# Performance work log

Measured on AMD Instinct MI355X. Metric: run time of the kernel, lower is better.

The kernel has to match this reference:

```python
import jax, jax.numpy as jnp
import numpy as np

EPS = 1e-5  # equinox LayerNorm default eps

def setup_inputs() -> dict:
    key = jax.random.key(0)
    k1, k2, k3, k4, k5 = jax.random.split(key, 5)
    heads, d, dH, N = 16, 1024, 64, 2048
    # lecun-normal-ish scaling for fan_in=d
    s = 1.0 / np.sqrt(d)
    return {
        "x": jax.random.normal(k1, (d, N), dtype=jnp.float32),
        "WQ": jax.random.normal(k2, (heads, d, dH), dtype=jnp.float32) * s,
        "WK": jax.random.normal(k3, (heads, d, dH), dtype=jnp.float32) * s,
        "WV": jax.random.normal(k4, (heads, d, dH), dtype=jnp.float32) * s,
        "W0": jax.random.normal(k5, (d, d), dtype=jnp.float32) * s,
    }

def reference(x, WQ, WK, WV, W0):
    # x: [d, N]
    residual = x
    # equinox LayerNorm over full shape (d, N), no affine params
    mean = jnp.mean(x)
    var = jnp.var(x)
    xn = (x - mean) * jax.lax.rsqrt(var + EPS)
    # project: [h, d_model, dH] x [d_model, N] -> [h, dH, N]
    Q = jnp.einsum('hcd,ci->hdi', WQ, xn)
    K = jnp.einsum('hcd,ci->hdi', WK, xn)
    V = jnp.einsum('hcd,ci->hdi', WV, xn)
    dH = WK.shape[-1]
    dot = jnp.einsum('hdi,hdj->hij', Q, K)  # [h, N, N]
    alpha = jax.nn.softmax(dot / jnp.sqrt(jnp.asarray(dH, dot.dtype)), axis=-1)
    attn = jnp.einsum('hij,hdj->hdi', alpha, V)  # [h, dH, N]
    N = attn.shape[2]
    attn = attn.reshape(-1, N)  # [d, N]
    out = W0 @ attn
    return out + residual
```

## Files before the change

### kernel.cpp

```cpp
#include <hip/hip_runtime.h>
#include <math.h>

typedef unsigned short u16;
typedef _Float16 f16;
typedef __attribute__((ext_vector_type(8))) short bf16x8;
typedef __attribute__((ext_vector_type(4))) float f32x4;
typedef __attribute__((ext_vector_type(4))) f16 f16x4;

#define D_MODEL 1024
#define SEQ_N   2048
#define HEADS   16
#define DHEAD   64
#define M3      3072
#define JSPLIT  2
#define JCHUNK  (SEQ_N / JSPLIT)
#define NIT     (JCHUNK / 64)

#define GLOBAL_AS __attribute__((address_space(1)))
#define LDS_AS    __attribute__((address_space(3)))
#define ASYNC16(gp, lp) __builtin_amdgcn_global_load_lds( \
    (const GLOBAL_AS unsigned int*)(gp), (LDS_AS unsigned int*)(lp), 16, 0, 0)

__device__ __forceinline__ u16 f2bf(float f) {
  union { float f; unsigned int u; } v; v.f = f;
  unsigned int r = v.u + 0x7fffu + ((v.u >> 16) & 1u);
  return (u16)(r >> 16);
}

__global__ __launch_bounds__(256) void ln_reduce1(const float* __restrict__ x,
                                                  double* __restrict__ part, int n4) {
  const float4* x4 = (const float4*)x;
  double s = 0.0, ss = 0.0;
  for (int idx = blockIdx.x * blockDim.x + threadIdx.x; idx < n4;
       idx += gridDim.x * blockDim.x) {
    float4 v = x4[idx];
    s  += (double)v.x + (double)v.y + (double)v.z + (double)v.w;
    ss += (double)v.x * v.x + (double)v.y * v.y + (double)v.z * v.z + (double)v.w * v.w;
  }
  __shared__ double ls[256], lss[256];
  int t = threadIdx.x;
  ls[t] = s; lss[t] = ss;
  __syncthreads();
  for (int off = 128; off > 0; off >>= 1) {
    if (t < off) { ls[t] += ls[t + off]; lss[t] += lss[t + off]; }
    __syncthreads();
  }
  if (t == 0) { part[2 * blockIdx.x] = ls[0]; part[2 * blockIdx.x + 1] = lss[0]; }
}

__global__ __launch_bounds__(256) void ln_norm_t(const float* __restrict__ x,
                                                 const double* __restrict__ part,
                                                 u16* __restrict__ xnt) {
  __shared__ double ls[256], lss[256];
  __shared__ float tile[64][65];
  int t = threadIdx.x;
  ls[t] = part[2 * t]; lss[t] = part[2 * t + 1];
  __syncthreads();
  for (int off = 128; off > 0; off >>= 1) {
    if (t < off) { ls[t] += ls[t + off]; lss[t] += lss[t + off]; }
    __syncthreads();
  }
  double inv = 1.0 / ((double)D_MODEL * (double)SEQ_N);
  double m = ls[0] * inv;
  double vv = lss[0] * inv - m * m;
  float mean = (float)m;
  float rstd = (float)(1.0 / sqrt(vv + 1e-5));

  int ib = blockIdx.x * 64, cb = blockIdx.y * 64;
  int il = t & 63, cl = t >> 6;
  for (int r = 0; r < 16; ++r) {
    int c = cl + r * 4;
    tile[c][il] = (x[(size_t)(cb + c) * SEQ_N + ib + il] - mean) * rstd;
  }
  __syncthreads();
  int c2 = t & 63, i2 = t >> 6;
  for (int r = 0; r < 16; ++r) {
    int i = i2 + r * 4;
    xnt[(size_t)(ib + i) * D_MODEL + cb + c2] = f2bf(tile[c2][i]);
  }
}

__global__ __launch_bounds__(256) void pack_w(const float* __restrict__ WQ,
                                              const float* __restrict__ WK,
                                              const float* __restrict__ WV,
                                              const float* __restrict__ W0,
                                              u16* __restrict__ Wp,
                                              u16* __restrict__ W0p) {
  int t = threadIdx.x;
  if (blockIdx.z == 3) {
    int flat = blockIdx.y * (D_MODEL / 32) + blockIdx.x;
    int idx = flat * 512 + t;
#pragma unroll
    for (int r = 0; r < 2; ++r, idx += 256) {
      float4 v = ((const float4*)W0)[idx];
      unsigned int lo = (unsigned int)f2bf(v.x) | ((unsigned int)f2bf(v.y) << 16);
      unsigned int hi = (unsigned int)f2bf(v.z) | ((unsigned int)f2bf(v.w) << 16);
      uint2 o; o.x = lo; o.y = hi;
      *(uint2*)(&W0p[(size_t)idx * 4]) = o;
    }
    return;
  }
  __shared__ float tile[32][65];
  const float* W = (blockIdx.z == 0) ? WQ : ((blockIdx.z == 1) ? WK : WV);
  int h = blockIdx.y, cb = blockIdx.x * 32;
  int dh = t & 63, cl = t >> 6;
  for (int r = 0; r < 8; ++r) {
    int c = cl + r * 4;
    tile[c][dh] = W[((size_t)h * D_MODEL + cb + c) * DHEAD + dh];
  }
  __syncthreads();
  int c2 = t & 31, d2 = t >> 5;
  for (int r = 0; r < 8; ++r) {
    int dd = d2 + r * 8;
    Wp[(size_t)((blockIdx.z * HEADS + h) * DHEAD + dd) * D_MODEL + cb + c2] =
        f2bf(tile[c2][dd]);
  }
}

__global__ __launch_bounds__(256) void gemm_qkv(const u16* __restrict__ A,
                                                const u16* __restrict__ Bt,
                                                u16* __restrict__ Qt,
                                                u16* __restrict__ Kt,
                                                f16* __restrict__ Vb) {
  __shared__ __align__(16) u16 Alds[2 * 96 * 32];
  __shared__ __align__(16) u16 Blds[2 * 128 * 32];
  int t = threadIdx.x;
  int lane = t & 63, w = t >> 6;
  int g = lane >> 4, l16 = lane & 15;
  int wr = w >> 1, wc = w & 1;
  int mb = blockIdx.y * 96, nb = blockIdx.x * 128;

  f32x4 acc[3][4];
#pragma unroll
  for (int i = 0; i < 3; ++i)
#pragma unroll
    for (int j = 0; j < 4; ++j) acc[i][j] = (f32x4){0.f, 0.f, 0.f, 0.f};

  const u16* AgP[3]; int ldsA[3];
#pragma unroll
  for (int r = 0; r < 3; ++r) {
    int idx = r * 256 + t;
    int kk = (idx >= 384) ? 1 : 0;
    int rem = idx - kk * 384;
    int row = rem >> 2, c4 = rem & 3;
    AgP[r] = A + (size_t)(mb + row) * D_MODEL + kk * 32 + c4 * 8;
    ldsA[r] = idx * 8;
  }
  const u16* BgP[4]; int ldsB[4];
#pragma unroll
  for (int r = 0; r < 4; ++r) {
    int idx = r * 256 + t;
    int kk = idx >> 9;
    int rem = idx & 511;
    int row = rem >> 2, c4 = rem & 3;
    BgP[r] = Bt + (size_t)(nb + row) * D_MODEL + kk * 32 + c4 * 8;
    ldsB[r] = idx * 8;
  }

  for (int kb = 0; kb < D_MODEL; kb += 64) {
#pragma unroll
    for (int r = 0; r < 3; ++r) ASYNC16(AgP[r] + kb, &Alds[ldsA[r]]);
#pragma unroll
    for (int r = 0; r < 4; ++r) ASYNC16(BgP[r] + kb, &Blds[ldsB[r]]);
    __syncthreads();
#pragma unroll
    for (int kk = 0; kk < 2; ++kk) {
      bf16x8 af[3], bf[4];
#pragma unroll
      for (int tm = 0; tm < 3; ++tm)
        af[tm] = *(const bf16x8*)(&Alds[kk * 3072 + (wr * 48 + tm * 16 + l16) * 32 + g * 8]);
#pragma unroll
      for (int tn = 0; tn < 4; ++tn)
        bf[tn] = *(const bf16x8*)(&Blds[kk * 4096 + (wc * 64 + tn * 16 + l16) * 32 + g * 8]);
#pragma unroll
      for (int tm = 0; tm < 3; ++tm)
#pragma unroll
        for (int tn = 0; tn < 4; ++tn)
          acc[tm][tn] = __builtin_amdgcn_mfma_f32_16x16x32_bf16(af[tm], bf[tn],
                                                                acc[tm][tn], 0, 0, 0);
    }
    __syncthreads();
  }

#pragma unroll
  for (int tm = 0; tm < 3; ++tm) {
    int row0 = mb + wr * 48 + tm * 16 + g * 4;
#pragma unroll
    for (int tn = 0; tn < 4; ++tn) {
      int col = nb + wc * 64 + tn * 16 + l16;
      if (row0 < 2 * D_MODEL) {
        u16* T = (row0 < D_MODEL) ? Qt : Kt;
        int rbase = (row0 < D_MODEL) ? row0 : row0 - D_MODEL;
        ushort4 o;
        o.x = f2bf(acc[tm][tn][0]); o.y = f2bf(acc[tm][tn][1]);
        o.z = f2bf(acc[tm][tn][2]); o.w = f2bf(acc[tm][tn][3]);
        *(ushort4*)(&T[(size_t)col * D_MODEL + rbase]) = o;
      } else {
        int rbase = row0 - 2 * D_MODEL;
#pragma unroll
        for (int r = 0; r < 4; ++r)
          Vb[(size_t)(rbase + r) * SEQ_N + col] = (f16)acc[tm][tn][r];
      }
    }
  }
}

__global__ __launch_bounds__(256) void gemm_bf16(const u16* __restrict__ A,
                                                 const u16* __restrict__ Bt,
                                                 float* __restrict__ C,
                                                 const float* __restrict__ res,
                                                 int M, int N, int K) {
  __shared__ __align__(16) u16 Alds[64 * 32];
  __shared__ __align__(16) u16 Blds[64 * 32];
  int t = threadIdx.x;
  int w = t >> 6, lane = t & 63;
  int g = lane >> 4, l16 = lane & 15;
  int mb = blockIdx.y * 64, nb = blockIdx.x * 64;
  f32x4 acc[4];
  for (int i = 0; i < 4; ++i) acc[i] = (f32x4){0.f, 0.f, 0.f, 0.f};
  int srow = t >> 2, scol = (t & 3) * 8;
  const u16* Ag = A + (size_t)(mb + srow) * K + scol;
  const u16* Bg = Bt + (size_t)(nb + srow) * K + scol;
  for (int kb = 0; kb < K; kb += 32) {
    ASYNC16(Ag + kb, &Alds[t * 8]);
    ASYNC16(Bg + kb, &Blds[t * 8]);
    __syncthreads();
    bf16x8 af = *(const bf16x8*)(&Alds[(w * 16 + l16) * 32 + g * 8]);
#pragma unroll
    for (int tn = 0; tn < 4; ++tn) {
      bf16x8 bf = *(const bf16x8*)(&Blds[(tn * 16 + l16) * 32 + g * 8]);
      acc[tn] = __builtin_amdgcn_mfma_f32_16x16x32_bf16(af, bf, acc[tn], 0, 0, 0);
    }
    __syncthreads();
  }
  int col0 = nb + l16;
  int row0 = mb + w * 16 + g * 4;
#pragma unroll
  for (int tn = 0; tn < 4; ++tn) {
    int col = col0 + tn * 16;
#pragma unroll
    for (int r = 0; r < 4; ++r) {
      int row = row0 + r;
      float v = acc[tn][r];
      if (res) v += res[(size_t)row * N + col];
      C[(size_t)row * N + col] = v;
    }
  }
}

__global__ __launch_bounds__(256, 2) void attn_mfma(const u16* __restrict__ Qt,
                                                    const u16* __restrict__ Kt,
                                                    const f16* __restrict__ Vb,
                                                    f16* __restrict__ Opart,
                                                    float* __restrict__ Lpart) {
  __shared__ __align__(16) u16 Klds[64][72];
  __shared__ __align__(16) f16 Vlds[64][72];
  int h = blockIdx.y;
  int ib = blockIdx.x * 128;
  int sp = blockIdx.z;
  int j0 = sp * JCHUNK;
  int t = threadIdx.x;
  int w = t >> 6, lane = t & 63;
  int g = lane >> 4, l16 = lane & 15;

  bf16x8 bq[2][2];
#pragma unroll
  for (int tm = 0; tm < 2; ++tm) {
    const u16* qb = Qt + (size_t)(ib + w * 32 + tm * 16 + l16) * D_MODEL + h * DHEAD + g * 8;
    bq[tm][0] = *(const bf16x8*)(qb);
    bq[tm][1] = *(const bf16x8*)(qb + 32);
  }

  f32x4 acc_o[2][4];
#pragma unroll
  for (int tm = 0; tm < 2; ++tm)
#pragma unroll
    for (int i = 0; i < 4; ++i) acc_o[tm][i] = (f32x4){0.f, 0.f, 0.f, 0.f};
  float lsum[2] = {0.f, 0.f};

  int srow = t >> 3, sch = (t & 7) * 8;
  const u16* Kg = Kt + (size_t)(j0 + srow) * D_MODEL + h * DHEAD + sch;
  const f16* Vg = Vb + (size_t)(h * DHEAD + srow) * SEQ_N + j0 + sch;

  uint4 kr0 = *(const uint4*)(Kg);
  uint4 kr1 = *(const uint4*)(Kg + 32 * (size_t)D_MODEL);
  uint4 vr0 = *(const uint4*)(Vg);
  uint4 vr1 = *(const uint4*)(Vg + 32 * (size_t)SEQ_N);

  for (int it = 0; it < NIT; ++it) {
    *(uint4*)(&Klds[srow][sch]) = kr0;
    *(uint4*)(&Klds[srow + 32][sch]) = kr1;
    *(uint4*)(&Vlds[srow][sch]) = vr0;
    *(uint4*)(&Vlds[srow + 32][sch]) = vr1;
    __syncthreads();

    if (it + 1 < NIT) {
      const u16* Kn = Kg + (size_t)(it + 1) * 64 * D_MODEL;
      const f16* Vn = Vg + (it + 1) * 64;
      kr0 = *(const uint4*)(Kn);
      kr1 = *(const uint4*)(Kn + 32 * (size_t)D_MODEL);
      vr0 = *(const uint4*)(Vn);
      vr1 = *(const uint4*)(Vn + 32 * (size_t)SEQ_N);
    }

    f32x4 s[2][4];
#pragma unroll
    for (int tm = 0; tm < 2; ++tm)
#pragma unroll
      for (int i = 0; i < 4; ++i) s[tm][i] = (f32x4){0.f, 0.f, 0.f, 0.f};
    __builtin_amdgcn_s_setprio(1);
#pragma unroll
    for (int kk = 0; kk < 2; ++kk)
#pragma unroll
      for (int tn = 0; tn < 4; ++tn) {
        bf16x8 ak = *(const bf16x8*)(&Klds[tn * 16 + l16][kk * 32 + g * 8]);
#pragma unroll
        for (int tm = 0; tm < 2; ++tm)
          s[tm][tn] = __builtin_amdgcn_mfma_f32_16x16x32_bf16(ak, bq[tm][kk],
                                                              s[tm][tn], 0, 0, 0);
      }
    __builtin_amdgcn_s_setprio(0);
    f16x4 pf[2][4];
#pragma unroll
    for (int tm = 0; tm < 2; ++tm)
#pragma unroll
      for (int tn = 0; tn < 4; ++tn)
#pragma unroll
        for (int r = 0; r < 4; ++r) {
          float pv = __expf(fmaf(s[tm][tn][r], 0.125f, -4.0f));
          lsum[tm] += pv;
          pf[tm][tn][r] = (f16)pv;
        }
    __builtin_amdgcn_s_setprio(1);
#pragma unroll
    for (int tn = 0; tn < 4; ++tn)
#pragma unroll
      for (int td = 0; td < 4; ++td) {
        f16x4 bv = *(const f16x4*)(&Vlds[td * 16 + l16][tn * 16 + g * 4]);
#pragma unroll
        for (int tm = 0; tm < 2; ++tm)
          acc_o[tm][td] =
              __builtin_amdgcn_mfma_f32_16x16x16f16(pf[tm][tn], bv, acc_o[tm][td], 0, 0, 0);
      }
    __builtin_amdgcn_s_setprio(0);
    __syncthreads();
  }

#pragma unroll
  for (int tm = 0; tm < 2; ++tm) {
    float l = lsum[tm];
    l += __shfl_xor(l, 16, 64);
    l += __shfl_xor(l, 32, 64);
    if (g == 0)
      Lpart[((size_t)sp * HEADS + h) * SEQ_N + ib + w * 32 + tm * 16 + l16] = l;
  }

#pragma unroll
  for (int tm = 0; tm < 2; ++tm)
#pragma unroll
    for (int td = 0; td < 4; ++td) {
      int dh = h * DHEAD + td * 16 + l16;
#pragma unroll
      for (int r = 0; r < 4; ++r) {
        int i = ib + w * 32 + tm * 16 + g * 4 + r;
        Opart[((size_t)sp * SEQ_N + i) * D_MODEL + dh] = (f16)acc_o[tm][td][r];
      }
    }
}

__global__ __launch_bounds__(256) void attn_combine(const f16* __restrict__ Opart,
                                                    const float* __restrict__ Lpart,
                                                    u16* __restrict__ attnt) {
  int i = blockIdx.x;
  int c = threadIdx.x * 4;
  int h = c >> 6;
  float l = 0.f;
#pragma unroll
  for (int s = 0; s < JSPLIT; ++s) l += Lpart[((size_t)s * HEADS + h) * SEQ_N + i];
  float o[4] = {0.f, 0.f, 0.f, 0.f};
#pragma unroll
  for (int s = 0; s < JSPLIT; ++s) {
    f16x4 v = *(const f16x4*)(&Opart[((size_t)s * SEQ_N + i) * D_MODEL + c]);
#pragma unroll
    for (int r = 0; r < 4; ++r) o[r] += (float)v[r];
  }
  float inv = 1.0f / l;
  ushort4 ob;
  ob.x = f2bf(o[0] * inv); ob.y = f2bf(o[1] * inv);
  ob.z = f2bf(o[2] * inv); ob.w = f2bf(o[3] * inv);
  *(ushort4*)(&attnt[(size_t)i * D_MODEL + c]) = ob;
}

extern "C" void kernel_launch(void* const* d_in, const int* in_sizes, int n_in,
                              void* d_out, int out_size, void* d_ws, size_t ws_size,
                              hipStream_t stream) {
  const float* x  = (const float*)d_in[0];
  const float* WQ = (const float*)d_in[1];
  const float* WK = (const float*)d_in[2];
  const float* WV = (const float*)d_in[3];
  const float* W0 = (const float*)d_in[4];
  float* out = (float*)d_out;

  char* ws = (char*)d_ws;
  size_t off = 0;
  double* part  = (double*)(ws + off); off += 8192;
  u16*    xnt   = (u16*)(ws + off); off += (size_t)SEQ_N * D_MODEL * 2;
  u16*    Wp    = (u16*)(ws + off); off += (size_t)M3 * D_MODEL * 2;
  u16*    W0p   = (u16*)(ws + off); off += (size_t)D_MODEL * D_MODEL * 2;
  u16*    Qt    = (u16*)(ws + off); off += (size_t)SEQ_N * D_MODEL * 2;
  u16*    Kt    = (u16*)(ws + off); off += (size_t)SEQ_N * D_MODEL * 2;
  f16*    Vb    = (f16*)(ws + off); off += (size_t)D_MODEL * SEQ_N * 2;
  u16*    attnt = (u16*)(ws + off); off += (size_t)SEQ_N * D_MODEL * 2;
  f16*    Opart = (f16*)(ws + off); off += (size_t)JSPLIT * SEQ_N * D_MODEL * 2;
  float*  Lpart = (float*)(ws + off); off += (size_t)JSPLIT * HEADS * SEQ_N * 4;

  ln_reduce1<<<256, 256, 0, stream>>>(x, part, (D_MODEL * SEQ_N) / 4);
  ln_norm_t<<<dim3(SEQ_N / 64, D_MODEL / 64), 256, 0, stream>>>(x, part, xnt);
  pack_w<<<dim3(D_MODEL / 32, HEADS, 4), 256, 0, stream>>>(WQ, WK, WV, W0, Wp, W0p);
  gemm_qkv<<<dim3(SEQ_N / 128, M3 / 96), 256, 0, stream>>>(Wp, xnt, Qt, Kt, Vb);
  attn_mfma<<<dim3(SEQ_N / 128, HEADS, JSPLIT), 256, 0, stream>>>(Qt, Kt, Vb, Opart, Lpart);
  attn_combine<<<SEQ_N, 256, 0, stream>>>(Opart, Lpart, attnt);
  gemm_bf16<<<dim3(SEQ_N / 64, D_MODEL / 64), 256, 0, stream>>>(W0p, attnt, out, x,
                                                                D_MODEL, SEQ_N, D_MODEL);
}
```

Measured before the change: 157.7 us.

## Double-buffer LDS in GEMMs and attention, merge prep kernels

Merges the layer-norm reduction and weight packing into a single launch to save one kernel launch. Adds LDS double buffering to the QKV GEMM, the output GEMM (now 64-wide K steps) and the attention K/V tiles, so loads for the next tile overlap compute and one barrier per iteration is dropped. The cost is twice the LDS footprint, which may reduce occupancy. Correctness relies on async global-to-LDS loads into the alternate buffer completing before the barrier that ends each iteration.

```diff
diff --git a/kernel.cpp b/kernel.cpp
--- a/kernel.cpp
+++ b/kernel.cpp
@@ -27,25 +27,64 @@
   return (u16)(r >> 16);
 }
 
-__global__ __launch_bounds__(256) void ln_reduce1(const float* __restrict__ x,
-                                                  double* __restrict__ part, int n4) {
-  const float4* x4 = (const float4*)x;
-  double s = 0.0, ss = 0.0;
-  for (int idx = blockIdx.x * blockDim.x + threadIdx.x; idx < n4;
-       idx += gridDim.x * blockDim.x) {
-    float4 v = x4[idx];
-    s  += (double)v.x + (double)v.y + (double)v.z + (double)v.w;
-    ss += (double)v.x * v.x + (double)v.y * v.y + (double)v.z * v.z + (double)v.w * v.w;
-  }
+__global__ __launch_bounds__(256) void prep(const float* __restrict__ x,
+                                            double* __restrict__ part,
+                                            const float* __restrict__ WQ,
+                                            const float* __restrict__ WK,
+                                            const float* __restrict__ WV,
+                                            const float* __restrict__ W0,
+                                            u16* __restrict__ Wp,
+                                            u16* __restrict__ W0p) {
   __shared__ double ls[256], lss[256];
+  __shared__ float tile[32][65];
   int t = threadIdx.x;
-  ls[t] = s; lss[t] = ss;
-  __syncthreads();
-  for (int off = 128; off > 0; off >>= 1) {
-    if (t < off) { ls[t] += ls[t + off]; lss[t] += lss[t + off]; }
+  int b = blockIdx.x;
+  if (b < 256) {
+    const float4* x4 = (const float4*)x;
+    const int n4 = (D_MODEL * SEQ_N) / 4;
+    double s = 0.0, ss = 0.0;
+    for (int idx = b * 256 + t; idx < n4; idx += 256 * 256) {
+      float4 v = x4[idx];
+      s  += (double)v.x + (double)v.y + (double)v.z + (double)v.w;
+      ss += (double)v.x * v.x + (double)v.y * v.y + (double)v.z * v.z + (double)v.w * v.w;
+    }
+    ls[t] = s; lss[t] = ss;
     __syncthreads();
-  }
-  if (t == 0) { part[2 * blockIdx.x] = ls[0]; part[2 * blockIdx.x + 1] = lss[0]; }
+    for (int off = 128; off > 0; off >>= 1) {
+      if (t < off) { ls[t] += ls[t + off]; lss[t] += lss[t + off]; }
+      __syncthreads();
+    }
+    if (t == 0) { part[2 * b] = ls[0]; part[2 * b + 1] = lss[0]; }
+    return;
+  }
+  int f = b - 256;
+  int z = f >> 9;
+  int rem = f & 511;
+  if (z == 3) {
+    int idx = rem * 512 + t;
+#pragma unroll
+    for (int r = 0; r < 2; ++r, idx += 256) {
+      float4 v = ((const float4*)W0)[idx];
+      unsigned int lo = (unsigned int)f2bf(v.x) | ((unsigned int)f2bf(v.y) << 16);
+      unsigned int hi = (unsigned int)f2bf(v.z) | ((unsigned int)f2bf(v.w) << 16);
+      uint2 o; o.x = lo; o.y = hi;
+      *(uint2*)(&W0p[(size_t)idx * 4]) = o;
+    }
+    return;
+  }
+  const float* W = (z == 0) ? WQ : ((z == 1) ? WK : WV);
+  int h = rem >> 5, cb = (rem & 31) * 32;
+  int dh = t & 63, cl = t >> 6;
+  for (int r = 0; r < 8; ++r) {
+    int c = cl + r * 4;
+    tile[c][dh] = W[((size_t)h * D_MODEL + cb + c) * DHEAD + dh];
+  }
+  __syncthreads();
+  int c2 = t & 31, d2 = t >> 5;
+  for (int r = 0; r < 8; ++r) {
+    int dd = d2 + r * 8;
+    Wp[(size_t)((z * HEADS + h) * DHEAD + dd) * D_MODEL + cb + c2] = f2bf(tile[c2][dd]);
+  }
 }
 
 __global__ __launch_bounds__(256) void ln_norm_t(const float* __restrict__ x,
@@ -80,50 +119,13 @@
   }
 }
 
-__global__ __launch_bounds__(256) void pack_w(const float* __restrict__ WQ,
-                                              const float* __restrict__ WK,
-                                              const float* __restrict__ WV,
-                                              const float* __restrict__ W0,
-                                              u16* __restrict__ Wp,
-                                              u16* __restrict__ W0p) {
-  int t = threadIdx.x;
-  if (blockIdx.z == 3) {
-    int flat = blockIdx.y * (D_MODEL / 32) + blockIdx.x;
-    int idx = flat * 512 + t;
-#pragma unroll
-    for (int r = 0; r < 2; ++r, idx += 256) {
-      float4 v = ((const float4*)W0)[idx];
-      unsigned int lo = (unsigned int)f2bf(v.x) | ((unsigned int)f2bf(v.y) << 16);
-      unsigned int hi = (unsigned int)f2bf(v.z) | ((unsigned int)f2bf(v.w) << 16);
-      uint2 o; o.x = lo; o.y = hi;
-      *(uint2*)(&W0p[(size_t)idx * 4]) = o;
-    }
-    return;
-  }
-  __shared__ float tile[32][65];
-  const float* W = (blockIdx.z == 0) ? WQ : ((blockIdx.z == 1) ? WK : WV);
-  int h = blockIdx.y, cb = blockIdx.x * 32;
-  int dh = t & 63, cl = t >> 6;
-  for (int r = 0; r < 8; ++r) {
-    int c = cl + r * 4;
-    tile[c][dh] = W[((size_t)h * D_MODEL + cb + c) * DHEAD + dh];
-  }
-  __syncthreads();
-  int c2 = t & 31, d2 = t >> 5;
-  for (int r = 0; r < 8; ++r) {
-    int dd = d2 + r * 8;
-    Wp[(size_t)((blockIdx.z * HEADS + h) * DHEAD + dd) * D_MODEL + cb + c2] =
-        f2bf(tile[c2][dd]);
-  }
-}
-
 __global__ __launch_bounds__(256) void gemm_qkv(const u16* __restrict__ A,
                                                 const u16* __restrict__ Bt,
                                                 u16* __restrict__ Qt,
                                                 u16* __restrict__ Kt,
                                                 f16* __restrict__ Vb) {
-  __shared__ __align__(16) u16 Alds[2 * 96 * 32];
-  __shared__ __align__(16) u16 Blds[2 * 128 * 32];
+  __shared__ __align__(16) u16 Alds[2 * 2 * 96 * 32];
+  __shared__ __align__(16) u16 Blds[2 * 2 * 128 * 32];
   int t = threadIdx.x;
   int lane = t & 63, w = t >> 6;
   int g = lane >> 4, l16 = lane & 15;
@@ -157,21 +159,33 @@
     ldsB[r] = idx * 8;
   }
 
-  for (int kb = 0; kb < D_MODEL; kb += 64) {
-#pragma unroll
-    for (int r = 0; r < 3; ++r) ASYNC16(AgP[r] + kb, &Alds[ldsA[r]]);
-#pragma unroll
-    for (int r = 0; r < 4; ++r) ASYNC16(BgP[r] + kb, &Blds[ldsB[r]]);
-    __syncthreads();
+#pragma unroll
+  for (int r = 0; r < 3; ++r) ASYNC16(AgP[r], &Alds[ldsA[r]]);
+#pragma unroll
+  for (int r = 0; r < 4; ++r) ASYNC16(BgP[r], &Blds[ldsB[r]]);
+  __syncthreads();
+
+  int cur = 0;
+  for (int ks = 0; ks < 16; ++ks) {
+    int nxt = cur ^ 1;
+    if (ks + 1 < 16) {
+      int kb = (ks + 1) * 64;
+#pragma unroll
+      for (int r = 0; r < 3; ++r) ASYNC16(AgP[r] + kb, &Alds[nxt * 6144 + ldsA[r]]);
+#pragma unroll
+      for (int r = 0; r < 4; ++r) ASYNC16(BgP[r] + kb, &Blds[nxt * 8192 + ldsB[r]]);
+    }
 #pragma unroll
     for (int kk = 0; kk < 2; ++kk) {
       bf16x8 af[3], bf[4];
 #pragma unroll
       for (int tm = 0; tm < 3; ++tm)
-        af[tm] = *(const bf16x8*)(&Alds[kk * 3072 + (wr * 48 + tm * 16 + l16) * 32 + g * 8]);
+        af[tm] = *(const bf16x8*)(&Alds[cur * 6144 + kk * 3072 +
+                                        (wr * 48 + tm * 16 + l16) * 32 + g * 8]);
 #pragma unroll
       for (int tn = 0; tn < 4; ++tn)
-        bf[tn] = *(const bf16x8*)(&Blds[kk * 4096 + (wc * 64 + tn * 16 + l16) * 32 + g * 8]);
+        bf[tn] = *(const bf16x8*)(&Blds[cur * 8192 + kk * 4096 +
+                                        (wc * 64 + tn * 16 + l16) * 32 + g * 8]);
 #pragma unroll
       for (int tm = 0; tm < 3; ++tm)
 #pragma unroll
@@ -180,6 +194,7 @@
                                                                 acc[tm][tn], 0, 0, 0);
     }
     __syncthreads();
+    cur = nxt;
   }
 
 #pragma unroll
@@ -210,28 +225,54 @@
                                                  float* __restrict__ C,
                                                  const float* __restrict__ res,
                                                  int M, int N, int K) {
-  __shared__ __align__(16) u16 Alds[64 * 32];
-  __shared__ __align__(16) u16 Blds[64 * 32];
+  __shared__ __align__(16) u16 Alds[2 * 2 * 64 * 32];
+  __shared__ __align__(16) u16 Blds[2 * 2 * 64 * 32];
   int t = threadIdx.x;
   int w = t >> 6, lane = t & 63;
   int g = lane >> 4, l16 = lane & 15;
   int mb = blockIdx.y * 64, nb = blockIdx.x * 64;
   f32x4 acc[4];
   for (int i = 0; i < 4; ++i) acc[i] = (f32x4){0.f, 0.f, 0.f, 0.f};
-  int srow = t >> 2, scol = (t & 3) * 8;
-  const u16* Ag = A + (size_t)(mb + srow) * K + scol;
-  const u16* Bg = Bt + (size_t)(nb + srow) * K + scol;
-  for (int kb = 0; kb < K; kb += 32) {
-    ASYNC16(Ag + kb, &Alds[t * 8]);
-    ASYNC16(Bg + kb, &Blds[t * 8]);
+
+  const u16* AgP[2]; const u16* BgP[2]; int ldsO[2];
+#pragma unroll
+  for (int r = 0; r < 2; ++r) {
+    int idx = r * 256 + t;
+    int kk = idx >> 8;
+    int rem = idx & 255;
+    int row = rem >> 2, c4 = rem & 3;
+    AgP[r] = A + (size_t)(mb + row) * K + kk * 32 + c4 * 8;
+    BgP[r] = Bt + (size_t)(nb + row) * K + kk * 32 + c4 * 8;
+    ldsO[r] = idx * 8;
+  }
+
+#pragma unroll
+  for (int r = 0; r < 2; ++r) { ASYNC16(AgP[r], &Alds[ldsO[r]]); ASYNC16(BgP[r], &Blds[ldsO[r]]); }
+  __syncthreads();
+
+  int cur = 0;
+  const int NK = 16;
+  for (int ks = 0; ks < NK; ++ks) {
+    int nxt = cur ^ 1;
+    if (ks + 1 < NK) {
+      int kb = (ks + 1) * 64;
+#pragma unroll
+      for (int r = 0; r < 2; ++r) {
+        ASYNC16(AgP[r] + kb, &Alds[nxt * 4096 + ldsO[r]]);
+        ASYNC16(BgP[r] + kb, &Blds[nxt * 4096 + ldsO[r]]);
+      }
+    }
+#pragma unroll
+    for (int kk = 0; kk < 2; ++kk) {
+      bf16x8 af = *(const bf16x8*)(&Alds[cur * 4096 + kk * 2048 + (w * 16 + l16) * 32 + g * 8]);
+#pragma unroll
+      for (int tn = 0; tn < 4; ++tn) {
+        bf16x8 bf = *(const bf16x8*)(&Blds[cur * 4096 + kk * 2048 + (tn * 16 + l16) * 32 + g * 8]);
+        acc[tn] = __builtin_amdgcn_mfma_f32_16x16x32_bf16(af, bf, acc[tn], 0, 0, 0);
+      }
+    }
     __syncthreads();
-    bf16x8 af = *(const bf16x8*)(&Alds[(w * 16 + l16) * 32 + g * 8]);
-#pragma unroll
-    for (int tn = 0; tn < 4; ++tn) {
-      bf16x8 bf = *(const bf16x8*)(&Blds[(tn * 16 + l16) * 32 + g * 8]);
-      acc[tn] = __builtin_amdgcn_mfma_f32_16x16x32_bf16(af, bf, acc[tn], 0, 0, 0);
-    }
-    __syncthreads();
+    cur = nxt;
   }
   int col0 = nb + l16;
   int row0 = mb + w * 16 + g * 4;
@@ -253,8 +294,8 @@
                                                     const f16* __restrict__ Vb,
                                                     f16* __restrict__ Opart,
                                                     float* __restrict__ Lpart) {
-  __shared__ __align__(16) u16 Klds[64][72];
-  __shared__ __align__(16) f16 Vlds[64][72];
+  __shared__ __align__(16) u16 Klds[2][64][72];
+  __shared__ __align__(16) f16 Vlds[2][64][72];
   int h = blockIdx.y;
   int ib = blockIdx.x * 128;
   int sp = blockIdx.z;
@@ -286,14 +327,14 @@
   uint4 kr1 = *(const uint4*)(Kg + 32 * (size_t)D_MODEL);
   uint4 vr0 = *(const uint4*)(Vg);
   uint4 vr1 = *(const uint4*)(Vg + 32 * (size_t)SEQ_N);
-
+  *(uint4*)(&Klds[0][srow][sch]) = kr0;
+  *(uint4*)(&Klds[0][srow + 32][sch]) = kr1;
+  *(uint4*)(&Vlds[0][srow][sch]) = vr0;
+  *(uint4*)(&Vlds[0][srow + 32][sch]) = vr1;
+  __syncthreads();
+
+  int cur = 0;
   for (int it = 0; it < NIT; ++it) {
-    *(uint4*)(&Klds[srow][sch]) = kr0;
-    *(uint4*)(&Klds[srow + 32][sch]) = kr1;
-    *(uint4*)(&Vlds[srow][sch]) = vr0;
-    *(uint4*)(&Vlds[srow + 32][sch]) = vr1;
-    __syncthreads();
-
     if (it + 1 < NIT) {
       const u16* Kn = Kg + (size_t)(it + 1) * 64 * D_MODEL;
       const f16* Vn = Vg + (it + 1) * 64;
@@ -313,7 +354,7 @@
     for (int kk = 0; kk < 2; ++kk)
 #pragma unroll
       for (int tn = 0; tn < 4; ++tn) {
-        bf16x8 ak = *(const bf16x8*)(&Klds[tn * 16 + l16][kk * 32 + g * 8]);
+        bf16x8 ak = *(const bf16x8*)(&Klds[cur][tn * 16 + l16][kk * 32 + g * 8]);
 #pragma unroll
         for (int tm = 0; tm < 2; ++tm)
           s[tm][tn] = __builtin_amdgcn_mfma_f32_16x16x32_bf16(ak, bq[tm][kk],
@@ -336,14 +377,22 @@
     for (int tn = 0; tn < 4; ++tn)
 #pragma unroll
       for (int td = 0; td < 4; ++td) {
-        f16x4 bv = *(const f16x4*)(&Vlds[td * 16 + l16][tn * 16 + g * 4]);
+        f16x4 bv = *(const f16x4*)(&Vlds[cur][td * 16 + l16][tn * 16 + g * 4]);
 #pragma unroll
         for (int tm = 0; tm < 2; ++tm)
           acc_o[tm][td] =
               __builtin_amdgcn_mfma_f32_16x16x16f16(pf[tm][tn], bv, acc_o[tm][td], 0, 0, 0);
       }
     __builtin_amdgcn_s_setprio(0);
+
+    if (it + 1 < NIT) {
+      *(uint4*)(&Klds[cur ^ 1][srow][sch]) = kr0;
+      *(uint4*)(&Klds[cur ^ 1][srow + 32][sch]) = kr1;
+      *(uint4*)(&Vlds[cur ^ 1][srow][sch]) = vr0;
+      *(uint4*)(&Vlds[cur ^ 1][srow + 32][sch]) = vr1;
+    }
     __syncthreads();
+    cur ^= 1;
   }
 
 #pragma unroll
@@ -414,9 +463,8 @@
   f16*    Opart = (f16*)(ws + off); off += (size_t)JSPLIT * SEQ_N * D_MODEL * 2;
   float*  Lpart = (float*)(ws + off); off += (size_t)JSPLIT * HEADS * SEQ_N * 4;
 
-  ln_reduce1<<<256, 256, 0, stream>>>(x, part, (D_MODEL * SEQ_N) / 4);
+  prep<<<256 + 2048, 256, 0, stream>>>(x, part, WQ, WK, WV, W0, Wp, W0p);
   ln_norm_t<<<dim3(SEQ_N / 64, D_MODEL / 64), 256, 0, stream>>>(x, part, xnt);
-  pack_w<<<dim3(D_MODEL / 32, HEADS, 4), 256, 0, stream>>>(WQ, WK, WV, W0, Wp, W0p);
   gemm_qkv<<<dim3(SEQ_N / 128, M3 / 96), 256, 0, stream>>>(Wp, xnt, Qt, Kt, Vb);
   attn_mfma<<<dim3(SEQ_N / 128, HEADS, JSPLIT), 256, 0, stream>>>(Qt, Kt, Vb, Opart, Lpart);
   attn_combine<<<SEQ_N, 256, 0, stream>>>(Opart, Lpart, attnt);
```

After: 155.0 us. About the same (-1.7%).
